# Performance work log

Hardware: AMD Instinct MI355X
Metric: run time of the kernel (lower is better)

## Reference

```python
import jax, jax.numpy as jnp
import numpy as np

M, IN, OUT = 8192, 4096, 4096
BITWIDTH = 7


def psto_shift_int32(x, shift):
    """Pseudo-stochastic right-shift of int32 x by `shift` bits -> int8.
    Faithful to PstoShiftInt32: floor-divide, derive a pseudo random number
    from the low half of the remainder, compare against the high half."""
    pow_s = jnp.left_shift(jnp.int32(1), shift)
    rt = jnp.floor_divide(x, pow_s)
    prob = jnp.abs(x - rt * pow_s)
    half_pow = jnp.left_shift(jnp.int32(1), shift // 2)
    qp = jnp.floor_divide(prob, half_pow)
    prn = prob - qp * half_pow
    prn = jnp.where(shift % 2 == 1, prn * 2, prn)
    dec = jnp.where(qp <= prn, jnp.int32(0), jnp.int32(1)) * jnp.sign(x)
    return jnp.clip(rt + dec, -127, 127).astype(jnp.int8)


def range_bitwidth(x):
    # RangeEstimate: ceil(log2(max|x|)), 0 if all-zero (torch also goes via float)
    m = jnp.max(jnp.abs(x)).astype(jnp.float32)
    return jnp.where(m == 0, jnp.int32(0), jnp.ceil(jnp.log2(m)).astype(jnp.int32))


def act_calc(acc, exp_in):
    """Shift int32 accumulator back to int8 and track the block exponent."""
    bw = range_bitwidth(acc)
    shift = bw - BITWIDTH
    # shift>1 -> shift by `shift`; shift==1 -> shift by 2; else -> plain int8 cast
    eff = jnp.where(shift > 1, shift, jnp.where(shift == 1, jnp.int32(2), jnp.int32(0)))
    rounded = psto_shift_int32(acc, jnp.maximum(eff, 0))
    out = jnp.where(eff > 0, rounded, acc.astype(jnp.int8))  # int8 cast wraps, as in torch
    exp_out = (exp_in + eff).astype(jnp.int8)
    return out, exp_out


def setup_inputs() -> dict:
    key = jax.random.key(0)
    k1, k2 = jax.random.split(key)
    # int8-valued tensors kept in int32 containers for the matmul accumulate
    act_in = jax.random.randint(k1, (M, IN), -127, 128, dtype=jnp.int32)
    weight = jax.random.randint(k2, (OUT, IN), -127, 128, dtype=jnp.int32)
    return {"act_in": act_in, "exp_in": -6, "weight": weight, "weight_exp": -9}


def reference(act_in, exp_in, weight, weight_exp):
    # the roundoff4 padding in the original is a no-op)
    acc = jnp.matmul(act_in, weight.T)  # [M, OUT] int32
    act_out, exp_out = act_calc(acc, jnp.int32(exp_in) + jnp.int32(weight_exp))
    return act_out, exp_out
```

## Files before the change

kernel.cpp:

```cpp
#include <hip/hip_runtime.h>
#include <stdint.h>
#include <math.h>

#define M_DIM 8192
#define N_DIM 4096
#define K_DIM 4096
#define BITWIDTH 7

#define BM 256
#define BN 128
#define NK 128

using i32x4  = __attribute__((ext_vector_type(4)))  int;
using i32x16 = __attribute__((ext_vector_type(16))) int;

#define FENCE asm volatile("" ::: "memory")

__global__ __launch_bounds__(256) void pack_both_kernel(
        const int* __restrict__ act, const int* __restrict__ wt,
        uint32_t* __restrict__ a8p, uint32_t* __restrict__ w8p,
        int* __restrict__ maxabs) {
    if (blockIdx.x == 0 && threadIdx.x == 0) *maxabs = 0;

    const int* src;
    uint32_t* dst;
    int t2;
    if (blockIdx.x < 8192) { src = act; dst = a8p; t2 = blockIdx.x * 256 + threadIdx.x; }
    else                   { src = wt;  dst = w8p; t2 = (blockIdx.x - 8192) * 256 + threadIdx.x; }

    const int L  = t2 & 63;
    const int kb = (t2 >> 6) & 127;
    const int rb = t2 >> 13;
    const size_t s = (size_t)(rb * 32 + (L & 31)) * K_DIM + kb * 32 + (L >> 5) * 16;
    const int4* sp = (const int4*)(src + s);
    uint32_t w[4];
#pragma unroll
    for (int q = 0; q < 4; ++q) {
        int4 v = sp[q];
        w[q] = (uint32_t)(v.x & 0xFF) | ((uint32_t)(v.y & 0xFF) << 8)
             | ((uint32_t)(v.z & 0xFF) << 16) | ((uint32_t)(v.w & 0xFF) << 24);
    }
    ((uint4*)dst)[t2] = make_uint4(w[0], w[1], w[2], w[3]);
}

__device__ __forceinline__ void load_af(i32x4 (&d)[2], const int8_t* aBase,
                                        int ks) {
#pragma unroll
    for (int i = 0; i < 2; ++i)
        d[i] = *(const i32x4*)(aBase + (size_t)((i * 128 + ks) << 10));
}

__device__ __forceinline__ void load_bfg(i32x4 (&d)[4], const int8_t* bBase,
                                         int ks) {
#pragma unroll
    for (int j = 0; j < 4; ++j)
        d[j] = *(const i32x4*)(bBase + (size_t)((j * 128 + ks) << 10));
}

__device__ __forceinline__ void kkstep(const i32x4 (&a)[2], const i32x4 (&b)[4],
                                       i32x16 (&acc)[2][4]) {
#pragma unroll
    for (int i = 0; i < 2; ++i)
#pragma unroll
        for (int j = 0; j < 4; ++j)
            acc[i][j] = __builtin_amdgcn_mfma_i32_32x32x32_i8(
                a[i], b[j], acc[i][j], 0, 0, 0);
}

__global__ __launch_bounds__(256, 2) void gemm_i8(
        const int8_t* __restrict__ A8p, const int8_t* __restrict__ B8p,
        int* __restrict__ C, int* __restrict__ maxabs) {
    __shared__ int wmaxs[4];

    const int tid  = threadIdx.x;
    const int wave = tid >> 6;
    const int lane = tid & 63;
    const int fr   = lane & 31;
    const int hl   = lane >> 5;

    const int row0 = blockIdx.y * BM;
    const int col0 = blockIdx.x * BN;
    const int wm   = wave * 64;

    i32x16 acc[2][4];
#pragma unroll
    for (int i = 0; i < 2; ++i)
#pragma unroll
        for (int j = 0; j < 4; ++j)
            acc[i][j] = (i32x16)(0);

    const int8_t* aBase = A8p + ((size_t)((row0 >> 5) + wave * 2) << 17)
                              + (size_t)lane * 16;
    const int8_t* bBase = B8p + ((size_t)(col0 >> 5) << 17)
                              + (size_t)lane * 16;

    i32x4 afE[2], afO[2], bfE[4], bfO[4];

    load_af(afE, aBase, 0);
    load_bfg(bfE, bBase, 0);

    for (int ks = 0; ks < NK; ks += 2) {
        load_af(afO, aBase, ks + 1);
        load_bfg(bfO, bBase, ks + 1);
        FENCE;
        kkstep(afE, bfE, acc);
        const int nxt = (ks + 2 < NK) ? ks + 2 : NK - 1;
        load_af(afE, aBase, nxt);
        load_bfg(bfE, bBase, nxt);
        FENCE;
        kkstep(afO, bfO, acc);
    }

    int mymax = 0;
    const int ccol = fr;
    const int rbase = hl << 2;
#pragma unroll
    for (int i = 0; i < 2; ++i) {
#pragma unroll
        for (int j = 0; j < 4; ++j) {
            int* p = C + (size_t)(row0 + wm + i * 32) * N_DIM
                       + (col0 + j * 32 + ccol);
#pragma unroll
            for (int r = 0; r < 16; ++r) {
                int row = (r & 3) + 8 * (r >> 2) + rbase;
                int v = acc[i][j][r];
                p[(size_t)row * N_DIM] = v;
                int a = v < 0 ? -v : v;
                mymax = a > mymax ? a : mymax;
            }
        }
    }

#pragma unroll
    for (int off = 32; off > 0; off >>= 1) {
        int o = __shfl_down(mymax, off, 64);
        mymax = o > mymax ? o : mymax;
    }
    if (lane == 0) wmaxs[wave] = mymax;
    __syncthreads();
    if (tid == 0) {
        int bmx = wmaxs[0];
        for (int w = 1; w < 4; ++w) bmx = wmaxs[w] > bmx ? wmaxs[w] : bmx;
        atomicMax(maxabs, bmx);
    }
}

__device__ __forceinline__ int psto(int x, int eff) {
    if (eff > 0) {
        int rt   = x >> eff;
        int prob = x & ((1 << eff) - 1);
        int h    = eff >> 1;
        int qp   = prob >> h;
        int prn  = (prob & ((1 << h) - 1)) << (eff & 1);
        int sgn  = (x > 0) - (x < 0);
        int r    = rt + ((qp <= prn) ? 0 : sgn);
        r = r < -127 ? -127 : r;
        r = r > 127 ? 127 : r;
        return r;
    }
    return (int)(int8_t)x;
}

__global__ __launch_bounds__(256) void finalize_kernel(int* __restrict__ C,
        const int* __restrict__ maxabs,
        const int* __restrict__ exp_in,
        const int* __restrict__ wexp) {
    const int m = *maxabs;
    int bw = 0;
    if (m != 0) bw = (int)ceilf(log2f((float)m));
    const int shift = bw - BITWIDTH;
    const int eff = (shift > 1) ? shift : ((shift == 1) ? 2 : 0);

    const size_t idx = ((size_t)blockIdx.x * blockDim.x + threadIdx.x) * 8;
    int4 v0 = *(const int4*)(C + idx);
    int4 v1 = *(const int4*)(C + idx + 4);
    int4 o0, o1;
    o0.x = psto(v0.x, eff); o0.y = psto(v0.y, eff);
    o0.z = psto(v0.z, eff); o0.w = psto(v0.w, eff);
    o1.x = psto(v1.x, eff); o1.y = psto(v1.y, eff);
    o1.z = psto(v1.z, eff); o1.w = psto(v1.w, eff);
    *(int4*)(C + idx) = o0;
    *(int4*)(C + idx + 4) = o1;

    if (idx == 0) {
        C[(size_t)M_DIM * N_DIM] = (int)(int8_t)(exp_in[0] + wexp[0] + eff);
    }
}

extern "C" void kernel_launch(void* const* d_in, const int* in_sizes, int n_in,
                              void* d_out, int out_size, void* d_ws, size_t ws_size,
                              hipStream_t stream) {
    const int* act    = (const int*)d_in[0];
    const int* exp_in = (const int*)d_in[1];
    const int* wt     = (const int*)d_in[2];
    const int* wexp   = (const int*)d_in[3];

    int8_t* a8p    = (int8_t*)d_ws;
    int8_t* w8p    = a8p + (size_t)M_DIM * K_DIM;
    int*    maxabs = (int*)(w8p + (size_t)N_DIM * K_DIM);

    pack_both_kernel<<<12288, 256, 0, stream>>>(
        act, wt, (uint32_t*)a8p, (uint32_t*)w8p, maxabs);

    int* C = (int*)d_out;
    dim3 grid(N_DIM / BN, M_DIM / BM);
    gemm_i8<<<grid, 256, 0, stream>>>(a8p, w8p, C, maxabs);

    finalize_kernel<<<((size_t)M_DIM * N_DIM / 8) / 256, 256, 0, stream>>>(
        C, maxabs, exp_in, wexp);
}
```

Before: 465.7 us.

## Stage B fragments in double-buffered LDS via global_load_lds, share across waves

Previously every wave loaded all four B fragments directly from global memory, so the four waves of a block fetched the same B data redundantly. Now each wave issues asynchronous global-to-LDS loads for one quarter of the B tile into a double-buffered shared array, and all waves read B from LDS. The K loop is restructured into 32 tiles of 4 k-steps, with explicit waitcnt/barrier sequencing and s_setprio around the MFMA blocks. This cuts global/L2 traffic for B but adds barriers and LDS reads, and relies on hand-tuned vmcnt counts that must match the issued loads.

```diff
diff --git a/kernel.cpp b/kernel.cpp
--- a/kernel.cpp
+++ b/kernel.cpp
@@ -9,7 +9,7 @@
 
 #define BM 256
 #define BN 128
-#define NK 128
+#define NT 32
 
 using i32x4  = __attribute__((ext_vector_type(4)))  int;
 using i32x16 = __attribute__((ext_vector_type(16))) int;
@@ -43,6 +43,13 @@
     ((uint4*)dst)[t2] = make_uint4(w[0], w[1], w[2], w[3]);
 }
 
+__device__ __forceinline__ void gload_lds16(const int8_t* g, int8_t* lds) {
+    __builtin_amdgcn_global_load_lds(
+        (__attribute__((address_space(1))) void*)g,
+        (__attribute__((address_space(3))) void*)lds,
+        16, 0, 0);
+}
+
 __device__ __forceinline__ void load_af(i32x4 (&d)[2], const int8_t* aBase,
                                         int ks) {
 #pragma unroll
@@ -50,11 +57,11 @@
         d[i] = *(const i32x4*)(aBase + (size_t)((i * 128 + ks) << 10));
 }
 
-__device__ __forceinline__ void load_bfg(i32x4 (&d)[4], const int8_t* bBase,
+__device__ __forceinline__ void load_bfl(i32x4 (&d)[4], const int8_t* bbuf,
                                          int ks) {
 #pragma unroll
     for (int j = 0; j < 4; ++j)
-        d[j] = *(const i32x4*)(bBase + (size_t)((j * 128 + ks) << 10));
+        d[j] = *(const i32x4*)(bbuf + ((j * 4 + ks) << 10));
 }
 
 __device__ __forceinline__ void kkstep(const i32x4 (&a)[2], const i32x4 (&b)[4],
@@ -70,7 +77,9 @@
 __global__ __launch_bounds__(256, 2) void gemm_i8(
         const int8_t* __restrict__ A8p, const int8_t* __restrict__ B8p,
         int* __restrict__ C, int* __restrict__ maxabs) {
+    __shared__ __align__(16) int8_t Bs[2][16384];
     __shared__ int wmaxs[4];
+    int8_t* BsF = &Bs[0][0];
 
     const int tid  = threadIdx.x;
     const int wave = tid >> 6;
@@ -91,24 +100,60 @@
 
     const int8_t* aBase = A8p + ((size_t)((row0 >> 5) + wave * 2) << 17)
                               + (size_t)lane * 16;
-    const int8_t* bBase = B8p + ((size_t)(col0 >> 5) << 17)
+    const int8_t* bSrc  = B8p + ((size_t)((col0 >> 5) + wave) << 17)
                               + (size_t)lane * 16;
 
-    i32x4 afE[2], afO[2], bfE[4], bfO[4];
-
-    load_af(afE, aBase, 0);
-    load_bfg(bfE, bBase, 0);
-
-    for (int ks = 0; ks < NK; ks += 2) {
-        load_af(afO, aBase, ks + 1);
-        load_bfg(bfO, bBase, ks + 1);
-        FENCE;
-        kkstep(afE, bfE, acc);
-        const int nxt = (ks + 2 < NK) ? ks + 2 : NK - 1;
-        load_af(afE, aBase, nxt);
-        load_bfg(bfE, bBase, nxt);
-        FENCE;
-        kkstep(afO, bfO, acc);
+    i32x4 af0[2], af1[2], af2[2], af3[2], bfA[4], bfB[4];
+
+#pragma unroll
+    for (int ks = 0; ks < 4; ++ks)
+        gload_lds16(bSrc + ((size_t)ks << 10), BsF + ((wave * 4 + ks) << 10));
+    FENCE;
+    load_af(af0, aBase, 0);
+    load_af(af1, aBase, 1);
+    asm volatile("s_waitcnt vmcnt(4)" ::: "memory");
+    __builtin_amdgcn_s_barrier();
+
+    for (int t = 0; t < NT; ++t) {
+        const int8_t* bbuf = BsF + ((t & 1) << 14) + (size_t)lane * 16;
+        int8_t* bstg = BsF + (((t + 1) & 1) << 14);
+        const bool st = (t < NT - 1);
+
+        load_bfl(bfA, bbuf, 0);
+        load_bfl(bfB, bbuf, 1);
+        FENCE;
+        load_af(af2, aBase, t * 4 + 2);
+        load_af(af3, aBase, t * 4 + 3);
+        FENCE;
+        if (st) {
+#pragma unroll
+            for (int ks = 0; ks < 4; ++ks)
+                gload_lds16(bSrc + ((size_t)((t + 1) * 4 + ks) << 10),
+                            bstg + ((wave * 4 + ks) << 10));
+        }
+        FENCE;
+        __builtin_amdgcn_s_barrier();
+        asm volatile("s_waitcnt lgkmcnt(0)" ::: "memory");
+        __builtin_amdgcn_s_setprio(1);
+        kkstep(af0, bfA, acc);
+        kkstep(af1, bfB, acc);
+        __builtin_amdgcn_s_setprio(0);
+        __builtin_amdgcn_s_barrier();
+
+        load_bfl(bfA, bbuf, 2);
+        load_bfl(bfB, bbuf, 3);
+        FENCE;
+        load_af(af0, aBase, st ? (t + 1) * 4 : 0);
+        load_af(af1, aBase, st ? (t + 1) * 4 + 1 : 1);
+        FENCE;
+        __builtin_amdgcn_s_barrier();
+        asm volatile("s_waitcnt lgkmcnt(0)" ::: "memory");
+        __builtin_amdgcn_s_setprio(1);
+        kkstep(af2, bfA, acc);
+        kkstep(af3, bfB, acc);
+        __builtin_amdgcn_s_setprio(0);
+        asm volatile("s_waitcnt vmcnt(4)" ::: "memory");
+        __builtin_amdgcn_s_barrier();
     }
 
     int mymax = 0;
```

Result: faster. 432.5 us (-7.1%).
